# Optimization experiments

Measured on AMD Instinct MI355X. Metric: run time of the kernel, lower is better.

Reference implementation:

```python
import jax, jax.numpy as jnp
import numpy as np

N, F, H, C, E = 50000, 256, 256, 40, 800000
CURV = 1.0
EPS = 4e-3      # hgcn PoincareBall eps for float32
MIN_NORM = 1e-15


def setup_inputs() -> dict:
    key = jax.random.key(0)
    ks = jax.random.split(key, 8)
    return {
        "x": jax.random.normal(ks[0], (N, F), jnp.float32),
        "edge_index": jax.random.randint(ks[1], (2, E), 0, N, dtype=jnp.int64),
        "Wl0": jax.random.normal(ks[2], (F, H), jnp.float32) / np.sqrt(F).astype(np.float32),
        "bl0": jnp.zeros((H,), jnp.float32),
        "Wr0": jax.random.normal(ks[3], (F, H), jnp.float32) / np.sqrt(F).astype(np.float32),
        "Wl1": jax.random.normal(ks[4], (H, C), jnp.float32) / np.sqrt(H).astype(np.float32),
        "bl1": jnp.zeros((C,), jnp.float32),
        "Wr1": jax.random.normal(ks[5], (H, C), jnp.float32) / np.sqrt(H).astype(np.float32),
        "W_lin": jax.random.normal(ks[6], (C * C, C), jnp.float32) / np.sqrt(C * C).astype(np.float32),
        "b_lin": jnp.zeros((C,), jnp.float32),
    }


def _sage(x, src, dst, Wl, bl, Wr):
    # PyG SAGEConv (mean aggr): lin_l(mean_{j->i} x_j) + lin_r(x_i), lin_l has bias
    msg = jax.ops.segment_sum(x[src], dst, num_segments=N)          # [N, d]
    cnt = jax.ops.segment_sum(jnp.ones((src.shape[0],), x.dtype), dst, num_segments=N)
    mean = msg / jnp.maximum(cnt, 1.0)[:, None]
    return mean @ Wl + bl + x @ Wr


def _proj(x, c):
    norm = jnp.maximum(jnp.linalg.norm(x, axis=-1, keepdims=True), MIN_NORM)
    maxnorm = (1.0 - EPS) / jnp.sqrt(c)
    return jnp.where(norm > maxnorm, x / norm * maxnorm, x)


def _logmap0(p, c):
    sqrt_c = jnp.sqrt(c)
    p_norm = jnp.maximum(jnp.linalg.norm(p, axis=-1, keepdims=True), MIN_NORM)
    arg = jnp.clip(sqrt_c * p_norm, -1.0 + 1e-6, 1.0 - 1e-6)
    return jnp.arctanh(arg) / (sqrt_c * p_norm) * p


def _expmap0(u, c):
    sqrt_c = jnp.sqrt(c)
    u_norm = jnp.maximum(jnp.linalg.norm(u, axis=-1, keepdims=True), MIN_NORM)
    return jnp.tanh(sqrt_c * u_norm) * u / (sqrt_c * u_norm)


def reference(x, edge_index, Wl0, bl0, Wr0, Wl1, bl1, Wr1, W_lin, b_lin):
    c = CURV
    src, dst = edge_index[0], edge_index[1]
    h = jax.nn.relu(_sage(x, src, dst, Wl0, bl0, Wr0))              # [N, H]
    h = _sage(h, src, dst, Wl1, bl1, Wr1)                            # [N, C]
    outer = jnp.einsum('ni,nj->nij', h, h).reshape(N, C * C)        # rank-1 outer, flattened
    h_hyp = _proj(outer, c)
    h_euc = _logmap0(h_hyp, c)                                       # proj_tan0 is identity
    h_euc = h_euc @ W_lin + b_lin                                    # [N, C]
    h_hyp = _proj(_expmap0(h_euc, c), c)
    return jax.nn.log_softmax(h_hyp, axis=-1)
```

## Files before the change

kernel.cpp:

```cpp
#include <hip/hip_runtime.h>
#include <math.h>


typedef short bf16x8 __attribute__((ext_vector_type(8)));
typedef float f32x4 __attribute__((ext_vector_type(4)));

#define AS1 __attribute__((address_space(1)))
#define AS3 __attribute__((address_space(3)))

__device__ inline unsigned pack_bf16_hu(float a, float b) {
    unsigned ua = __float_as_uint(a) + 0x8000u;
    unsigned ub = __float_as_uint(b) + 0x8000u;
    return __builtin_amdgcn_perm(ub, ua, 0x07060302u);
}

__device__ inline unsigned short f2bf_rne(float x) {
    unsigned u = __float_as_uint(x);
    unsigned r = (u + 0x7fffu + ((u >> 16) & 1u)) >> 16;
    return (unsigned short)r;
}

__device__ inline void split2(float a, float b, unsigned* hw, unsigned* lw) {
    unsigned ua = __float_as_uint(a) + 0x8000u;
    unsigned ub = __float_as_uint(b) + 0x8000u;
    *hw = __builtin_amdgcn_perm(ub, ua, 0x07060302u);
    float ra = a - __uint_as_float(ua & 0xFFFF0000u);
    float rb = b - __uint_as_float(ub & 0xFFFF0000u);
    unsigned va = __float_as_uint(ra) + 0x8000u;
    unsigned vb = __float_as_uint(rb) + 0x8000u;
    *lw = __builtin_amdgcn_perm(vb, va, 0x07060302u);
}


__global__ void k_count(const int* __restrict__ dst, int* __restrict__ deg, int E) {
    int e = blockIdx.x * 256 + threadIdx.x;
    if (e < E) atomicAdd(&deg[dst[e]], 1);
}

__global__ __launch_bounds__(256) void k_scanA(const int* __restrict__ deg,
                                               int* __restrict__ offs,
                                               float* __restrict__ invc,
                                               int* __restrict__ bsum, int N) {
    __shared__ int wt[4];
    int tid = threadIdx.x, lane = tid & 63, wid = tid >> 6;
    int base = blockIdx.x * 1024 + tid * 4;
    int v[4];
    #pragma unroll
    for (int j = 0; j < 4; ++j) {
        int i = base + j;
        v[j] = (i < N) ? deg[i] : 0;
        if (i < N) invc[i] = 1.0f / (float)max(v[j], 1);
    }
    int t = v[0] + v[1] + v[2] + v[3];
    int s = t;
    #pragma unroll
    for (int d = 1; d < 64; d <<= 1) {
        int u = __shfl_up(s, d);
        if (lane >= d) s += u;
    }
    if (lane == 63) wt[wid] = s;
    __syncthreads();
    int wpre = 0, btot = 0;
    #pragma unroll
    for (int q = 0; q < 4; ++q) {
        int x = wt[q];
        btot += x;
        if (q < wid) wpre += x;
    }
    int run = wpre + s - t;
    #pragma unroll
    for (int j = 0; j < 4; ++j) {
        int i = base + j;
        if (i < N) offs[i] = run;
        run += v[j];
    }
    if (tid == 0) bsum[blockIdx.x] = btot;
}

__global__ __launch_bounds__(64) void k_scanB(int* __restrict__ bsum,
                                              int* __restrict__ offs, int N, int G) {
    int lane = threadIdx.x;
    int run = 0;
    for (int base = 0; base < G; base += 64) {
        int i = base + lane;
        int v = (i < G) ? bsum[i] : 0;
        int s = v;
        #pragma unroll
        for (int d = 1; d < 64; d <<= 1) {
            int u = __shfl_up(s, d);
            if (lane >= d) s += u;
        }
        int tot = __shfl(s, 63);
        if (i < G) bsum[i] = run + s - v;
        run += tot;
    }
    if (lane == 0) offs[N] = run;
}

__global__ __launch_bounds__(256) void k_scanC(int* __restrict__ offs,
                                               const int* __restrict__ bsum, int N) {
    int add = bsum[blockIdx.x];
    int base = blockIdx.x * 1024 + threadIdx.x * 4;
    #pragma unroll
    for (int j = 0; j < 4; ++j) {
        int i = base + j;
        if (i < N) offs[i] += add;
    }
}

__global__ void k_scatter(const int* __restrict__ src, const int* __restrict__ dst,
                          const int* __restrict__ offs, int* __restrict__ cursor,
                          int* __restrict__ ssrc, int E) {
    int e = blockIdx.x * 256 + threadIdx.x;
    if (e >= E) return;
    int d = dst[e];
    int pos = offs[d] + atomicAdd(&cursor[d], 1);
    ssrc[pos] = src[e];
}


__global__ __launch_bounds__(256) void k_wsplit0(const float* __restrict__ Wl,
                                                 const float* __restrict__ Wr,
                                                 unsigned short* __restrict__ Wth,
                                                 unsigned short* __restrict__ Wtl) {
    int idx = blockIdx.x * 256 + threadIdx.x;
    int n = idx >> 8, k = idx & 255;
    float v = (n < 256) ? Wl[k * 256 + n] : Wr[k * 256 + (n - 256)];
    unsigned short h = f2bf_rne(v);
    float hf = __uint_as_float(((unsigned)h) << 16);
    Wth[idx] = h;
    Wtl[idx] = f2bf_rne(v - hf);
}

__global__ __launch_bounds__(256) void k_wsplit1(const float* __restrict__ Wl,
                                                 const float* __restrict__ Wr,
                                                 unsigned short* __restrict__ Wth,
                                                 unsigned short* __restrict__ Wtl) {
    int idx = blockIdx.x * 256 + threadIdx.x;
    if (idx >= 80 * 256) return;
    int n = idx >> 8, k = idx & 255;
    float v = (n < 40) ? Wl[k * 40 + n] : Wr[k * 40 + (n - 40)];
    unsigned short h = f2bf_rne(v);
    float hf = __uint_as_float(((unsigned)h) << 16);
    Wth[idx] = h;
    Wtl[idx] = f2bf_rne(v - hf);
}


__global__ __launch_bounds__(256) void k_xsplit(const float* __restrict__ X,
                                                unsigned short* __restrict__ Xh,
                                                unsigned short* __restrict__ Xl,
                                                int N) {
    int idx = blockIdx.x * 256 + threadIdx.x;
    int n = idx >> 5, c = idx & 31;
    float4 v0 = make_float4(0.f, 0.f, 0.f, 0.f);
    float4 v1 = make_float4(0.f, 0.f, 0.f, 0.f);
    if (n < N) {
        v0 = *(const float4*)&X[(size_t)n * 256 + c * 8];
        v1 = *(const float4*)&X[(size_t)n * 256 + c * 8 + 4];
    }
    unsigned h0, l0, h1, l1, h2, l2, h3, l3;
    split2(v0.x, v0.y, &h0, &l0);
    split2(v0.z, v0.w, &h1, &l1);
    split2(v1.x, v1.y, &h2, &l2);
    split2(v1.z, v1.w, &h3, &l3);
    int cp = c ^ (n & 7);
    size_t o = (size_t)n * 256 + cp * 8;
    *(uint4*)&Xh[o] = make_uint4(h0, h1, h2, h3);
    *(uint4*)&Xl[o] = make_uint4(l0, l1, l2, l3);
}


__global__ __launch_bounds__(512) void gemm0_mfma(const unsigned short* __restrict__ Xh,
                                                  const unsigned short* __restrict__ Xl,
                                                  const unsigned short* __restrict__ Bh,
                                                  const unsigned short* __restrict__ Bl,
                                                  unsigned short* __restrict__ Yl,
                                                  float* __restrict__ Yr, int N) {
    __shared__ __align__(16) unsigned short AhL[64 * 256];
    __shared__ __align__(16) unsigned short AlL[64 * 256];

    int tid = threadIdx.x;
    int lane = tid & 63;
    int w = __builtin_amdgcn_readfirstlane(tid >> 6);
    int ml = lane & 15, quad = lane >> 4;
    int m0 = blockIdx.x * 64;
    bool isYl = (w < 4);
    int wc = w & 3;

    {
        const char* gh = (const char*)Xh + (size_t)m0 * 512;
        const char* gl = (const char*)Xl + (size_t)m0 * 512;
        #pragma unroll
        for (int j = 0; j < 4; ++j) {
            int off = (j * 512 + tid) * 16;
            __builtin_amdgcn_global_load_lds((const AS1 unsigned*)(gh + off),
                                             (AS3 unsigned*)((char*)AhL + off), 16, 0, 0);
            __builtin_amdgcn_global_load_lds((const AS1 unsigned*)(gl + off),
                                             (AS3 unsigned*)((char*)AlL + off), 16, 0, 0);
        }
    }

    f32x4 acc[4][4];
    #pragma unroll
    for (int a = 0; a < 4; ++a)
        #pragma unroll
        for (int b = 0; b < 4; ++b) acc[a][b] = (f32x4){0.f, 0.f, 0.f, 0.f};

    int bcol[4];
    #pragma unroll
    for (int nf = 0; nf < 4; ++nf)
        bcol[nf] = isYl ? (wc * 64 + (nf & 2) * 16 + 2 * ml + (nf & 1))
                        : (256 + wc * 64 + nf * 16 + ml);

    bf16x8 bh0[4], bl0[4], bh1[4], bl1[4];

    auto loadB = [&](int it, bf16x8* bh, bf16x8* bl) {
        int ko = it * 32 + quad * 8;
        #pragma unroll
        for (int nf = 0; nf < 4; ++nf) {
            size_t bo = (size_t)bcol[nf] * 256 + ko;
            bh[nf] = *(const bf16x8*)&Bh[bo];
            bl[nf] = *(const bf16x8*)&Bl[bo];
        }
    };

    loadB(0, bh0, bl0);
    __syncthreads();

    const char* AhB = (const char*)AhL;
    const char* AlB = (const char*)AlL;
    int swz = ml & 7;

    #pragma unroll
    for (int g = 0; g < 8; ++g) {
        bf16x8* bhc = (g & 1) ? bh1 : bh0;
        bf16x8* blc = (g & 1) ? bl1 : bl0;
        bf16x8* bhn = (g & 1) ? bh0 : bh1;
        bf16x8* bln = (g & 1) ? bl0 : bl1;
        if (g < 7) loadB(g + 1, bhn, bln);
        bf16x8 ah[4], al[4];
        #pragma unroll
        for (int mf = 0; mf < 4; ++mf) {
            int ro = (mf * 16 + ml) * 512 + (((g * 4 + quad) ^ swz) * 16);
            ah[mf] = *(const bf16x8*)(AhB + ro);
            al[mf] = *(const bf16x8*)(AlB + ro);
        }
        #pragma unroll
        for (int nf = 0; nf < 4; ++nf)
            #pragma unroll
            for (int mf = 0; mf < 4; ++mf) {
                acc[mf][nf] = __builtin_amdgcn_mfma_f32_16x16x32_bf16(ah[mf], bhc[nf], acc[mf][nf], 0, 0, 0);
                acc[mf][nf] = __builtin_amdgcn_mfma_f32_16x16x32_bf16(ah[mf], blc[nf], acc[mf][nf], 0, 0, 0);
                acc[mf][nf] = __builtin_amdgcn_mfma_f32_16x16x32_bf16(al[mf], bhc[nf], acc[mf][nf], 0, 0, 0);
            }
    }

    if (isYl) {
        #pragma unroll
        for (int mf = 0; mf < 4; ++mf)
            #pragma unroll
            for (int r = 0; r < 4; ++r) {
                int row = m0 + mf * 16 + quad * 4 + r;
                if (row < N) {
                    unsigned p0 = pack_bf16_hu(acc[mf][0][r], acc[mf][1][r]);
                    unsigned p1 = pack_bf16_hu(acc[mf][2][r], acc[mf][3][r]);
                    *(unsigned*)&Yl[(size_t)row * 256 + wc * 64 + 2 * ml] = p0;
                    *(unsigned*)&Yl[(size_t)row * 256 + wc * 64 + 32 + 2 * ml] = p1;
                }
            }
    } else {
        #pragma unroll
        for (int mf = 0; mf < 4; ++mf)
            #pragma unroll
            for (int r = 0; r < 4; ++r) {
                int row = m0 + mf * 16 + quad * 4 + r;
                if (row < N) {
                    #pragma unroll
                    for (int nf = 0; nf < 4; ++nf)
                        Yr[(size_t)row * 256 + wc * 64 + nf * 16 + ml] = acc[mf][nf][r];
                }
            }
    }
}


__global__ __launch_bounds__(256) void combine0(const unsigned short* __restrict__ Yl,
                                                const float* __restrict__ Yr,
                                                const int* __restrict__ offs,
                                                const int* __restrict__ ssrc,
                                                const float* __restrict__ invc,
                                                const float* __restrict__ bl0,
                                                unsigned short* __restrict__ Hh,
                                                unsigned short* __restrict__ Hl, int N) {
    int wv = threadIdx.x >> 6, lane = threadIdx.x & 63;
    int n = blockIdx.x * 4 + wv;
    if (n >= N) return;
    int e0 = offs[n], e1 = offs[n + 1];
    float4 acc = make_float4(0.f, 0.f, 0.f, 0.f);
    int e = e0;
    for (; e + 3 < e1; e += 4) {
        int s0 = ssrc[e], s1 = ssrc[e + 1], s2 = ssrc[e + 2], s3 = ssrc[e + 3];
        uint2 p = *(const uint2*)&Yl[(size_t)s0 * 256 + lane * 4];
        uint2 q = *(const uint2*)&Yl[(size_t)s1 * 256 + lane * 4];
        uint2 u = *(const uint2*)&Yl[(size_t)s2 * 256 + lane * 4];
        uint2 t = *(const uint2*)&Yl[(size_t)s3 * 256 + lane * 4];
        acc.x += (__uint_as_float(p.x << 16) + __uint_as_float(q.x << 16)) +
                 (__uint_as_float(u.x << 16) + __uint_as_float(t.x << 16));
        acc.y += (__uint_as_float(p.x & 0xFFFF0000u) + __uint_as_float(q.x & 0xFFFF0000u)) +
                 (__uint_as_float(u.x & 0xFFFF0000u) + __uint_as_float(t.x & 0xFFFF0000u));
        acc.z += (__uint_as_float(p.y << 16) + __uint_as_float(q.y << 16)) +
                 (__uint_as_float(u.y << 16) + __uint_as_float(t.y << 16));
        acc.w += (__uint_as_float(p.y & 0xFFFF0000u) + __uint_as_float(q.y & 0xFFFF0000u)) +
                 (__uint_as_float(u.y & 0xFFFF0000u) + __uint_as_float(t.y & 0xFFFF0000u));
    }
    for (; e < e1; ++e) {
        int s0 = ssrc[e];
        uint2 p = *(const uint2*)&Yl[(size_t)s0 * 256 + lane * 4];
        acc.x += __uint_as_float(p.x << 16);
        acc.y += __uint_as_float(p.x & 0xFFFF0000u);
        acc.z += __uint_as_float(p.y << 16);
        acc.w += __uint_as_float(p.y & 0xFFFF0000u);
    }
    float ic = invc[n];
    float4 b = *(const float4*)&bl0[lane * 4];
    float4 yr = *(const float4*)&Yr[(size_t)n * 256 + lane * 4];
    float hx = fmaxf(acc.x * ic + b.x + yr.x, 0.f);
    float hy = fmaxf(acc.y * ic + b.y + yr.y, 0.f);
    float hz = fmaxf(acc.z * ic + b.z + yr.z, 0.f);
    float hw = fmaxf(acc.w * ic + b.w + yr.w, 0.f);
    unsigned h0, h1, l0, l1;
    split2(hx, hy, &h0, &l0);
    split2(hz, hw, &h1, &l1);
    int t2 = n >> 4, r = n & 15;
    int kc = lane >> 3, q = (lane >> 1) & 3, ee = (lane & 1) * 4;
    size_t offH = (size_t)t2 * 4096 + kc * 512 + q * 128 + r * 8 + ee;
    *(uint2*)&Hh[offH] = make_uint2(h0, h1);
    *(uint2*)&Hl[offH] = make_uint2(l0, l1);
}


__global__ __launch_bounds__(256) void gemm1_mfma(const unsigned short* __restrict__ Hh,
                                                  const unsigned short* __restrict__ Hl,
                                                  const unsigned short* __restrict__ Bh,
                                                  const unsigned short* __restrict__ Bl,
                                                  unsigned short* __restrict__ Zl,
                                                  float* __restrict__ Zr, int N, int numTiles) {
    int tid = threadIdx.x;
    int lane = tid & 63;
    int w = __builtin_amdgcn_readfirstlane(tid >> 6);
    int ml = lane & 15, quad = lane >> 4;
    int t = blockIdx.x * 4 + w;
    if (t >= numTiles) return;

    const unsigned short* ahp = Hh + (size_t)t * 4096 + quad * 128 + ml * 8;
    const unsigned short* alp = Hl + (size_t)t * 4096 + quad * 128 + ml * 8;

    f32x4 acc[5];
    #pragma unroll
    for (int b = 0; b < 5; ++b) acc[b] = (f32x4){0.f, 0.f, 0.f, 0.f};

    #pragma unroll
    for (int kc = 0; kc < 8; ++kc) {
        bf16x8 ah = *(const bf16x8*)&ahp[kc * 512];
        bf16x8 al = *(const bf16x8*)&alp[kc * 512];
        int ko = kc * 32 + quad * 8;
        #pragma unroll
        for (int nf = 0; nf < 5; ++nf) {
            size_t bo = (size_t)(nf * 16 + ml) * 256 + ko;
            bf16x8 bh = *(const bf16x8*)&Bh[bo];
            bf16x8 bl = *(const bf16x8*)&Bl[bo];
            acc[nf] = __builtin_amdgcn_mfma_f32_16x16x32_bf16(ah, bh, acc[nf], 0, 0, 0);
            acc[nf] = __builtin_amdgcn_mfma_f32_16x16x32_bf16(ah, bl, acc[nf], 0, 0, 0);
            acc[nf] = __builtin_amdgcn_mfma_f32_16x16x32_bf16(al, bh, acc[nf], 0, 0, 0);
        }
    }
    #pragma unroll
    for (int r = 0; r < 4; ++r) {
        int n = t * 16 + quad * 4 + r;
        if (n < N) {
            #pragma unroll
            for (int nf = 0; nf < 5; ++nf) {
                int col = nf * 16 + ml;
                if (col < 40) Zl[(size_t)n * 40 + col] = f2bf_rne(acc[nf][r]);
                else Zr[(size_t)n * 40 + (col - 40)] = acc[nf][r];
            }
        }
    }
}


__global__ __launch_bounds__(256) void combine1(const unsigned short* __restrict__ Zl,
                                                const float* __restrict__ Zr,
                                                const int* __restrict__ offs,
                                                const int* __restrict__ ssrc,
                                                const float* __restrict__ invc,
                                                const float* __restrict__ bl1,
                                                float* __restrict__ H2, int N) {
    int wv = threadIdx.x >> 6, lane = threadIdx.x & 63;
    int n = blockIdx.x * 4 + wv;
    if (n >= N) return;
    if (lane >= 40) return;
    int e0 = offs[n], e1 = offs[n + 1];
    float acc = 0.f;
    int e = e0;
    for (; e + 1 < e1; e += 2) {
        int s0 = ssrc[e], s1 = ssrc[e + 1];
        unsigned a = Zl[(size_t)s0 * 40 + lane];
        unsigned b = Zl[(size_t)s1 * 40 + lane];
        acc += __uint_as_float(a << 16) + __uint_as_float(b << 16);
    }
    if (e < e1) {
        unsigned a = Zl[(size_t)ssrc[e] * 40 + lane];
        acc += __uint_as_float(a << 16);
    }
    float v = acc * invc[n] + bl1[lane] + Zr[(size_t)n * 40 + lane];
    H2[(size_t)n * 40 + lane] = v;
}


__global__ __launch_bounds__(256) void k_wprep(const float* __restrict__ W,
                                               unsigned short* __restrict__ WbF) {
    int idx = blockIdx.x * 256 + threadIdx.x;
    if (idx >= 180 * 64) return;
    int slot = idx >> 6, lane = idx & 63;
    int cf = slot % 3;
    int cs = slot / 3;
    int s = cs % 3;
    int c = cs / 3;
    int ml = lane & 15, quad = lane >> 4;
    int col = cf * 16 + ml;
    int kbase = c * 96 + s * 32 + quad * 8;
    unsigned short v8[8];
    #pragma unroll
    for (int e = 0; e < 8; ++e) {
        int kp = kbase + e;
        int i = kp / 48;
        int j = kp - i * 48;
        float v = 0.f;
        if (col < 40 && i < 40 && j < 40) v = W[((size_t)(i * 40 + j)) * 40 + col];
        v8[e] = f2bf_rne(v);
    }
    *(uint4*)&WbF[(size_t)idx * 8] = *(uint4*)v8;
}


__global__ __launch_bounds__(256, 1) void k_final_mfma(const float* __restrict__ H2,
                                                       const unsigned short* __restrict__ WbF,
                                                       const float* __restrict__ blin,
                                                       float* __restrict__ out, int N) {
    int tid = threadIdx.x;
    int m0 = blockIdx.x * 64;
    int lane = tid & 63;
    int w = __builtin_amdgcn_readfirstlane(tid >> 6);
    int ml = lane & 15;
    int quad = lane >> 4;
    int row = w * 16 + ml;
    int gn = m0 + row;

    float g[48];
    float s2 = 0.f;
    #pragma unroll
    for (int q4 = 0; q4 < 10; ++q4) {
        float4 v = make_float4(0.f, 0.f, 0.f, 0.f);
        if (gn < N) v = *(const float4*)&H2[(size_t)gn * 40 + q4 * 4];
        g[q4 * 4 + 0] = v.x; g[q4 * 4 + 1] = v.y;
        g[q4 * 4 + 2] = v.z; g[q4 * 4 + 3] = v.w;
        s2 += v.x * v.x + v.y * v.y + v.z * v.z + v.w * v.w;
    }
    #pragma unroll
    for (int j = 40; j < 48; ++j) g[j] = 0.f;

    float aln = atanhf(fminf(fmaxf(s2, 1e-15f), 0.996f)) / fmaxf(s2, 1e-30f);

    bool isQ0 = (quad == 0), isQ2 = (quad == 2), qLo = (quad < 2);
    float wA[8], wB[8], wC[8];
    #pragma unroll
    for (int j = 0; j < 8; ++j) {
        float a0 = isQ0 ? g[j] : g[8 + j];
        float a1 = isQ2 ? g[16 + j] : g[24 + j];
        wA[j] = qLo ? a0 : a1;
        float b0 = isQ0 ? g[32 + j] : g[40 + j];
        float b1 = isQ2 ? g[j] : g[8 + j];
        wB[j] = qLo ? b0 : b1;
        float c0 = isQ0 ? g[16 + j] : g[24 + j];
        float c1 = isQ2 ? g[32 + j] : g[40 + j];
        wC[j] = qLo ? c0 : c1;
    }

    f32x4 acc[3];
    #pragma unroll
    for (int c = 0; c < 3; ++c) acc[c] = (f32x4){0.f, 0.f, 0.f, 0.f};

    const unsigned short* bw = WbF + (size_t)lane * 8;

    #pragma unroll
    for (int c = 0; c < 20; ++c) {
        float gi0 = g[2 * c];
        float gi1 = qLo ? g[2 * c] : g[2 * c + 1];
        float gi2 = g[2 * c + 1];
        {
            const int slot = (c * 3 + 0) * 3;
            union { unsigned u[4]; bf16x8 v; } A;
            A.u[0] = pack_bf16_hu(gi0 * wA[0], gi0 * wA[1]);
            A.u[1] = pack_bf16_hu(gi0 * wA[2], gi0 * wA[3]);
            A.u[2] = pack_bf16_hu(gi0 * wA[4], gi0 * wA[5]);
            A.u[3] = pack_bf16_hu(gi0 * wA[6], gi0 * wA[7]);
            #pragma unroll
            for (int cf = 0; cf < 3; ++cf) {
                bf16x8 bf = *(const bf16x8*)&bw[(size_t)(slot + cf) * 512];
                acc[cf] = __builtin_amdgcn_mfma_f32_16x16x32_bf16(A.v, bf, acc[cf], 0, 0, 0);
            }
        }
        {
            const int slot = (c * 3 + 1) * 3;
            union { unsigned u[4]; bf16x8 v; } A;
            A.u[0] = pack_bf16_hu(gi1 * wB[0], gi1 * wB[1]);
            A.u[1] = pack_bf16_hu(gi1 * wB[2], gi1 * wB[3]);
            A.u[2] = pack_bf16_hu(gi1 * wB[4], gi1 * wB[5]);
            A.u[3] = pack_bf16_hu(gi1 * wB[6], gi1 * wB[7]);
            #pragma unroll
            for (int cf = 0; cf < 3; ++cf) {
                bf16x8 bf = *(const bf16x8*)&bw[(size_t)(slot + cf) * 512];
                acc[cf] = __builtin_amdgcn_mfma_f32_16x16x32_bf16(A.v, bf, acc[cf], 0, 0, 0);
            }
        }
        {
            const int slot = (c * 3 + 2) * 3;
            union { unsigned u[4]; bf16x8 v; } A;
            A.u[0] = pack_bf16_hu(gi2 * wC[0], gi2 * wC[1]);
            A.u[1] = pack_bf16_hu(gi2 * wC[2], gi2 * wC[3]);
            A.u[2] = pack_bf16_hu(gi2 * wC[4], gi2 * wC[5]);
            A.u[3] = pack_bf16_hu(gi2 * wC[6], gi2 * wC[7]);
            #pragma unroll
            for (int cf = 0; cf < 3; ++cf) {
                bf16x8 bf = *(const bf16x8*)&bw[(size_t)(slot + cf) * 512];
                acc[cf] = __builtin_amdgcn_mfma_f32_16x16x32_bf16(A.v, bf, acc[cf], 0, 0, 0);
            }
        }
    }

    float bcol[3];
    #pragma unroll
    for (int c = 0; c < 3; ++c) {
        int col = c * 16 + ml;
        bcol[c] = (col < 40) ? blin[col] : 0.f;
    }
    bool v2 = (ml < 8);

    #pragma unroll
    for (int r = 0; r < 4; ++r) {
        int nloc = w * 16 + quad * 4 + r;
        float al = __shfl(aln, quad * 4 + r);
        float u0 = al * acc[0][r] + bcol[0];
        float u1 = al * acc[1][r] + bcol[1];
        float u2 = v2 ? (al * acc[2][r] + bcol[2]) : 0.f;
        float un2 = u0 * u0 + u1 * u1 + u2 * u2;
        #pragma unroll
        for (int m = 1; m < 16; m <<= 1) un2 += __shfl_xor(un2, m);
        float un = fmaxf(sqrtf(un2), 1e-15f);
        float tnh = tanhf(un);
        float gma = tnh / un;
        float ps = (tnh > 0.996f) ? (0.996f / tnh) : 1.0f;
        float s = gma * ps;
        float l0 = s * u0, l1 = s * u1, l2 = s * u2;
        float mx = fmaxf(l0, l1);
        if (v2) mx = fmaxf(mx, l2);
        #pragma unroll
        for (int m = 1; m < 16; m <<= 1) mx = fmaxf(mx, __shfl_xor(mx, m));
        float se = expf(l0 - mx) + expf(l1 - mx) + (v2 ? expf(l2 - mx) : 0.f);
        #pragma unroll
        for (int m = 1; m < 16; m <<= 1) se += __shfl_xor(se, m);
        float lse = logf(se);
        int go = m0 + nloc;
        if (go < N) {
            out[(size_t)go * 40 + ml] = l0 - mx - lse;
            out[(size_t)go * 40 + 16 + ml] = l1 - mx - lse;
            if (v2) out[(size_t)go * 40 + 32 + ml] = l2 - mx - lse;
        }
    }
}


extern "C" void kernel_launch(void* const* d_in, const int* in_sizes, int n_in,
                              void* d_out, int out_size, void* d_ws, size_t ws_size,
                              hipStream_t stream) {
    const float* x    = (const float*)d_in[0];
    const int*   ei   = (const int*)d_in[1];
    const float* Wl0  = (const float*)d_in[2];
    const float* bl0  = (const float*)d_in[3];
    const float* Wr0  = (const float*)d_in[4];
    const float* Wl1  = (const float*)d_in[5];
    const float* bl1  = (const float*)d_in[6];
    const float* Wr1  = (const float*)d_in[7];
    const float* Wlin = (const float*)d_in[8];
    const float* blin = (const float*)d_in[9];
    int N = in_sizes[0] / 256;
    int E = in_sizes[1] / 2;
    const int* src = ei;
    const int* dst = ei + E;
    int numTiles = (N + 15) / 16;
    int Npad = ((N + 63) / 64) * 64;

    char* ws = (char*)d_ws;
    size_t off = 0;
    auto carve = [&](size_t bytes) -> char* {
        char* p = ws + off;
        off = (off + bytes + 255) & ~(size_t)255;
        return p;
    };
    size_t xbytes = (size_t)Npad * 256 * 2;
    int*   deg    = (int*)carve((size_t)N * 4);
    int*   cursor = (int*)carve((size_t)N * 4);
    int*   offs   = (int*)carve((size_t)(N + 1) * 4);
    float* invc   = (float*)carve((size_t)N * 4);
    int*   bsum   = (int*)carve(1024);
    int*   ssrc   = (int*)carve((size_t)E * 4);
    unsigned short* Yl = (unsigned short*)carve((size_t)N * 256 * 2);
    float* Yr     = (float*)carve((size_t)N * 256 * 4);
    unsigned short* Hh = (unsigned short*)carve(xbytes);
    unsigned short* Hl = (unsigned short*)carve(xbytes);
    unsigned short* Zl = (unsigned short*)carve((size_t)N * 40 * 2);
    float* Zr     = (float*)carve((size_t)N * 40 * 4);
    float* H2     = (float*)carve((size_t)N * 40 * 4);
    unsigned short* Xh = Hh;
    unsigned short* Xl = Hl;
    unsigned short* Wb = (unsigned short*)Yr;
    unsigned short* Wth  = (unsigned short*)H2;
    unsigned short* Wtl  = Wth + 512 * 256;
    unsigned short* Wt1h = Wtl + 512 * 256;
    unsigned short* Wt1l = Wt1h + 80 * 256;

    int G = (N + 1023) / 1024;

    hipMemsetAsync(deg, 0, (size_t)N * 4, stream);
    hipMemsetAsync(cursor, 0, (size_t)N * 4, stream);

    k_count<<<(E + 255) / 256, 256, 0, stream>>>(dst, deg, E);
    k_scanA<<<G, 256, 0, stream>>>(deg, offs, invc, bsum, N);
    k_scanB<<<1, 64, 0, stream>>>(bsum, offs, N, G);
    k_scanC<<<G, 256, 0, stream>>>(offs, bsum, N);
    k_scatter<<<(E + 255) / 256, 256, 0, stream>>>(src, dst, offs, cursor, ssrc, E);
    k_wsplit0<<<(512 * 256) / 256, 256, 0, stream>>>(Wl0, Wr0, Wth, Wtl);
    k_wsplit1<<<(80 * 256 + 255) / 256, 256, 0, stream>>>(Wl1, Wr1, Wt1h, Wt1l);
    k_xsplit<<<(Npad * 32) / 256, 256, 0, stream>>>(x, Xh, Xl, N);
    gemm0_mfma<<<(N + 63) / 64, 512, 0, stream>>>(Xh, Xl, Wth, Wtl, Yl, Yr, N);
    combine0<<<(N + 3) / 4, 256, 0, stream>>>(Yl, Yr, offs, ssrc, invc, bl0, Hh, Hl, N);
    k_wprep<<<(180 * 64 + 255) / 256, 256, 0, stream>>>(Wlin, Wb);
    gemm1_mfma<<<(numTiles + 3) / 4, 256, 0, stream>>>(Hh, Hl, Wt1h, Wt1l, Zl, Zr, N, numTiles);
    combine1<<<(N + 3) / 4, 256, 0, stream>>>(Zl, Zr, offs, ssrc, invc, bl1, H2, N);
    k_final_mfma<<<(N + 63) / 64, 256, 0, stream>>>(H2, Wb, blin, (float*)d_out, N);
}
```

Measured before the change: 477.8 us.

## Halve gemm0 row tile and double-buffer the K-halves of the A tile in LDS

The first-layer GEMM now processes 32 rows per block instead of 64 and splits the A tile along K into two LDS buffers. The second half is loaded while the first half is being computed. B fragments are loaded inline per K step rather than register double-buffered, and launch bounds request higher occupancy. The aim is to cut LDS per block, raise occupancy and overlap the global-to-LDS copy with MFMA work. The trade-off is that each B fragment is reused across fewer rows, so B traffic per output row doubles.

```diff
diff --git a/kernel.cpp b/kernel.cpp
--- a/kernel.cpp
+++ b/kernel.cpp
@@ -171,39 +171,38 @@
 }
 
 
-__global__ __launch_bounds__(512) void gemm0_mfma(const unsigned short* __restrict__ Xh,
-                                                  const unsigned short* __restrict__ Xl,
-                                                  const unsigned short* __restrict__ Bh,
-                                                  const unsigned short* __restrict__ Bl,
-                                                  unsigned short* __restrict__ Yl,
-                                                  float* __restrict__ Yr, int N) {
-    __shared__ __align__(16) unsigned short AhL[64 * 256];
-    __shared__ __align__(16) unsigned short AlL[64 * 256];
+__global__ __launch_bounds__(512, 4) void gemm0_mfma(const unsigned short* __restrict__ Xh,
+                                                     const unsigned short* __restrict__ Xl,
+                                                     const unsigned short* __restrict__ Bh,
+                                                     const unsigned short* __restrict__ Bl,
+                                                     unsigned short* __restrict__ Yl,
+                                                     float* __restrict__ Yr, int N) {
+    __shared__ __align__(16) unsigned short AhL[2][32 * 128];
+    __shared__ __align__(16) unsigned short AlL[2][32 * 128];
 
     int tid = threadIdx.x;
     int lane = tid & 63;
     int w = __builtin_amdgcn_readfirstlane(tid >> 6);
     int ml = lane & 15, quad = lane >> 4;
-    int m0 = blockIdx.x * 64;
+    int m0 = blockIdx.x * 32;
     bool isYl = (w < 4);
     int wc = w & 3;
 
-    {
-        const char* gh = (const char*)Xh + (size_t)m0 * 512;
-        const char* gl = (const char*)Xl + (size_t)m0 * 512;
-        #pragma unroll
-        for (int j = 0; j < 4; ++j) {
-            int off = (j * 512 + tid) * 16;
-            __builtin_amdgcn_global_load_lds((const AS1 unsigned*)(gh + off),
-                                             (AS3 unsigned*)((char*)AhL + off), 16, 0, 0);
-            __builtin_amdgcn_global_load_lds((const AS1 unsigned*)(gl + off),
-                                             (AS3 unsigned*)((char*)AlL + off), 16, 0, 0);
-        }
-    }
-
-    f32x4 acc[4][4];
-    #pragma unroll
-    for (int a = 0; a < 4; ++a)
+    auto stage = [&](int buf, int p) {
+        int row = tid >> 4, c16 = tid & 15;
+        size_t gsrc = (size_t)(m0 + row) * 512 + (size_t)p * 256 + c16 * 16;
+        int off = tid * 16;
+        __builtin_amdgcn_global_load_lds((const AS1 unsigned*)((const char*)Xh + gsrc),
+                                         (AS3 unsigned*)((char*)&AhL[buf][0] + off), 16, 0, 0);
+        __builtin_amdgcn_global_load_lds((const AS1 unsigned*)((const char*)Xl + gsrc),
+                                         (AS3 unsigned*)((char*)&AlL[buf][0] + off), 16, 0, 0);
+    };
+
+    stage(0, 0);
+
+    f32x4 acc[2][4];
+    #pragma unroll
+    for (int a = 0; a < 2; ++a)
         #pragma unroll
         for (int b = 0; b < 4; ++b) acc[a][b] = (f32x4){0.f, 0.f, 0.f, 0.f};
 
@@ -213,52 +212,47 @@
         bcol[nf] = isYl ? (wc * 64 + (nf & 2) * 16 + 2 * ml + (nf & 1))
                         : (256 + wc * 64 + nf * 16 + ml);
 
-    bf16x8 bh0[4], bl0[4], bh1[4], bl1[4];
-
-    auto loadB = [&](int it, bf16x8* bh, bf16x8* bl) {
-        int ko = it * 32 + quad * 8;
-        #pragma unroll
-        for (int nf = 0; nf < 4; ++nf) {
-            size_t bo = (size_t)bcol[nf] * 256 + ko;
-            bh[nf] = *(const bf16x8*)&Bh[bo];
-            bl[nf] = *(const bf16x8*)&Bl[bo];
-        }
-    };
-
-    loadB(0, bh0, bl0);
+    int swz = ml & 7;
     __syncthreads();
 
-    const char* AhB = (const char*)AhL;
-    const char* AlB = (const char*)AlL;
-    int swz = ml & 7;
-
-    #pragma unroll
-    for (int g = 0; g < 8; ++g) {
-        bf16x8* bhc = (g & 1) ? bh1 : bh0;
-        bf16x8* blc = (g & 1) ? bl1 : bl0;
-        bf16x8* bhn = (g & 1) ? bh0 : bh1;
-        bf16x8* bln = (g & 1) ? bl0 : bl1;
-        if (g < 7) loadB(g + 1, bhn, bln);
-        bf16x8 ah[4], al[4];
-        #pragma unroll
-        for (int mf = 0; mf < 4; ++mf) {
-            int ro = (mf * 16 + ml) * 512 + (((g * 4 + quad) ^ swz) * 16);
-            ah[mf] = *(const bf16x8*)(AhB + ro);
-            al[mf] = *(const bf16x8*)(AlB + ro);
-        }
-        #pragma unroll
-        for (int nf = 0; nf < 4; ++nf)
-            #pragma unroll
-            for (int mf = 0; mf < 4; ++mf) {
-                acc[mf][nf] = __builtin_amdgcn_mfma_f32_16x16x32_bf16(ah[mf], bhc[nf], acc[mf][nf], 0, 0, 0);
-                acc[mf][nf] = __builtin_amdgcn_mfma_f32_16x16x32_bf16(ah[mf], blc[nf], acc[mf][nf], 0, 0, 0);
-                acc[mf][nf] = __builtin_amdgcn_mfma_f32_16x16x32_bf16(al[mf], bhc[nf], acc[mf][nf], 0, 0, 0);
-            }
+    #pragma unroll
+    for (int p = 0; p < 2; ++p) {
+        if (p == 0) stage(1, 1);
+        const char* base_h = (const char*)&AhL[p][0];
+        const char* base_l = (const char*)&AlL[p][0];
+        #pragma unroll
+        for (int g2 = 0; g2 < 4; ++g2) {
+            int g = p * 4 + g2;
+            int ko = g * 32 + quad * 8;
+            bf16x8 bh[4], bl[4];
+            #pragma unroll
+            for (int nf = 0; nf < 4; ++nf) {
+                size_t bo = (size_t)bcol[nf] * 256 + ko;
+                bh[nf] = *(const bf16x8*)&Bh[bo];
+                bl[nf] = *(const bf16x8*)&Bl[bo];
+            }
+            bf16x8 ah[2], al[2];
+            #pragma unroll
+            for (int mf = 0; mf < 2; ++mf) {
+                int ro = (mf * 16 + ml) * 256 + (((g2 * 4 + quad) ^ swz) * 16);
+                ah[mf] = *(const bf16x8*)(base_h + ro);
+                al[mf] = *(const bf16x8*)(base_l + ro);
+            }
+            #pragma unroll
+            for (int nf = 0; nf < 4; ++nf)
+                #pragma unroll
+                for (int mf = 0; mf < 2; ++mf) {
+                    acc[mf][nf] = __builtin_amdgcn_mfma_f32_16x16x32_bf16(ah[mf], bh[nf], acc[mf][nf], 0, 0, 0);
+                    acc[mf][nf] = __builtin_amdgcn_mfma_f32_16x16x32_bf16(ah[mf], bl[nf], acc[mf][nf], 0, 0, 0);
+                    acc[mf][nf] = __builtin_amdgcn_mfma_f32_16x16x32_bf16(al[mf], bh[nf], acc[mf][nf], 0, 0, 0);
+                }
+        }
+        if (p == 0) __syncthreads();
     }
 
     if (isYl) {
         #pragma unroll
-        for (int mf = 0; mf < 4; ++mf)
+        for (int mf = 0; mf < 2; ++mf)
             #pragma unroll
             for (int r = 0; r < 4; ++r) {
                 int row = m0 + mf * 16 + quad * 4 + r;
@@ -271,7 +265,7 @@
             }
     } else {
         #pragma unroll
-        for (int mf = 0; mf < 4; ++mf)
+        for (int mf = 0; mf < 2; ++mf)
             #pragma unroll
             for (int r = 0; r < 4; ++r) {
                 int row = m0 + mf * 16 + quad * 4 + r;
@@ -644,7 +638,7 @@
     k_wsplit0<<<(512 * 256) / 256, 256, 0, stream>>>(Wl0, Wr0, Wth, Wtl);
     k_wsplit1<<<(80 * 256 + 255) / 256, 256, 0, stream>>>(Wl1, Wr1, Wt1h, Wt1l);
     k_xsplit<<<(Npad * 32) / 256, 256, 0, stream>>>(x, Xh, Xl, N);
-    gemm0_mfma<<<(N + 63) / 64, 512, 0, stream>>>(Xh, Xl, Wth, Wtl, Yl, Yr, N);
+    gemm0_mfma<<<(N + 31) / 32, 512, 0, stream>>>(Xh, Xl, Wth, Wtl, Yl, Yr, N);
     combine0<<<(N + 3) / 4, 256, 0, stream>>>(Yl, Yr, offs, ssrc, invc, bl0, Hh, Hl, N);
     k_wprep<<<(180 * 64 + 255) / 256, 256, 0, stream>>>(Wlin, Wb);
     gemm1_mfma<<<(numTiles + 3) / 4, 256, 0, stream>>>(Hh, Hl, Wt1h, Wt1l, Zl, Zr, N, numTiles);
```

New measurement: 506.0 us. 1.06x slower.
